# Kernel tuning notes

Measured on AMD Instinct MI355X. Metric: run time of the kernel, lower is better.

Reference implementation:

```python
import jax, jax.numpy as jnp
import numpy as np


def setup_inputs() -> dict:
    key = jax.random.key(0)
    B, M, L = 65536, 64, 256  # frames, LPC order, analysis window length
    # Build valid autocorrelation sequences (positive-definite Toeplitz)
    # from random signals via FFT: r_k = sum_t x_t x_{t+k}.
    x = jax.random.normal(key, (B, L), dtype=jnp.float32)
    spec = jnp.abs(jnp.fft.rfft(x, n=2 * L, axis=-1)) ** 2
    r = jnp.fft.irfft(spec, n=2 * L, axis=-1)[..., : M + 1] / L
    # small diagonal loading for numerical safety of the solve / sqrt
    r = r.at[..., 0].add(1e-3)
    return {"r": r.astype(jnp.float32)}


def reference(r):
    # r: (..., M+1) autocorrelation. out_format == 'Ka'.
    M = r.shape[-1] - 1
    # Symmetric Toeplitz R[i, j] = r[|i - j|] built by gathering lags.
    idx = jnp.abs(jnp.arange(M)[:, None] - jnp.arange(M)[None, :])  # (M, M)
    R = r[..., :-1][..., idx]  # (..., M, M)
    r1 = r[..., 1:]  # (..., M)
    # a = R^{-1} (-r1); solve is the efficient form of inverse @ vec (same math).
    a = jnp.linalg.solve(R, -r1[..., None])[..., 0]  # (..., M)
    r0 = r[..., 0]
    K = jnp.sqrt(jnp.einsum("...m,...m->...", r1, a) + r0)[..., None]  # (..., 1)
    return jnp.concatenate((K, a), axis=-1)  # (..., M+1)
```

## Files before the change

kernel.cpp:

```cpp
#include <hip/hip_runtime.h>
#include <math.h>


constexpr int M  = 64;
constexpr int EL = M + 1;
constexpr int BT = 128;

__global__ __launch_bounds__(BT) void levinson_kernel(const float* __restrict__ rin,
                                                      float* __restrict__ out,
                                                      int B) {
  __shared__ float smem[BT * EL];
  const int tid = threadIdx.x;
  const int b0  = blockIdx.x * BT;
  const int nb  = min(BT, B - b0);
  const int nf  = nb * EL;
  const size_t base = (size_t)b0 * EL;

  {
    const int n4 = nf >> 2;
    const float4* in4 = reinterpret_cast<const float4*>(rin + base);
    float4* s4 = reinterpret_cast<float4*>(smem);
    for (int i = tid; i < n4; i += BT) s4[i] = in4[i];
    for (int i = (n4 << 2) + tid; i < nf; i += BT) smem[i] = rin[base + i];
  }
  __syncthreads();

  float K = 0.f;
  float a[M + 1];
  if (tid < nb) {
    float r[EL];
#pragma unroll
    for (int i = 0; i < EL; ++i) r[i] = smem[tid * EL + i];

    float Eacc = r[0];
#pragma unroll
    for (int m = 1; m <= M; ++m) {
      float s[4] = {0.f, 0.f, 0.f, 0.f};
#pragma unroll
      for (int j = 1; j <= m - 1; ++j)
        s[j & 3] = fmaf(a[j], r[m - j], s[j & 3]);
      const float acc = r[m] + ((s[0] + s[1]) + (s[2] + s[3]));
      const float k = -acc / Eacc;
#pragma unroll
      for (int j = 1; 2 * j < m; ++j) {
        const float aj = a[j], amj = a[m - j];
        a[j]     = fmaf(k, amj, aj);
        a[m - j] = fmaf(k, aj, amj);
      }
      if ((m & 1) == 0) {
        const float ah = a[m >> 1];
        a[m >> 1] = fmaf(k, ah, ah);
      }
      a[m] = k;
      Eacc = fmaf(-k * k, Eacc, Eacc);
    }
    K = sqrtf(Eacc);
  }

  if (tid < nb) {
    smem[tid * EL] = K;
#pragma unroll
    for (int j = 1; j <= M; ++j) smem[tid * EL + j] = a[j];
  }
  __syncthreads();

  {
    const int n4 = nf >> 2;
    const float4* s4 = reinterpret_cast<const float4*>(smem);
    float4* out4 = reinterpret_cast<float4*>(out + base);
    for (int i = tid; i < n4; i += BT) out4[i] = s4[i];
    for (int i = (n4 << 2) + tid; i < nf; i += BT) out[base + i] = smem[i];
  }
}

extern "C" void kernel_launch(void* const* d_in, const int* in_sizes, int n_in,
                              void* d_out, int out_size, void* d_ws, size_t ws_size,
                              hipStream_t stream) {
  const float* r = (const float*)d_in[0];
  float* out = (float*)d_out;
  const int B = in_sizes[0] / EL;
  const int blocks = (B + BT - 1) / BT;
  levinson_kernel<<<blocks, BT, 0, stream>>>(r, out, B);
}
```

Measured before the change: 91.59 us.

## Reformulate Levinson recursion with fixed-length forward/backward polynomials and rolled outer loop

Replaces the triangular Levinson update, whose inner loops have lengths that depend on m and so force a full unroll of the outer loop, with a lattice formulation. It keeps a forward polynomial A and a backward polynomial Bb and runs fixed-length 64-wide dot and update loops every iteration, so the outer loop can stay rolled with register-resident arrays. This cuts instruction-cache pressure and code size, at the cost of about twice the FMAs, since each step always processes the full order instead of only m terms. The block size also drops to 64 threads with launch_bounds(…,1), which allows more registers per thread.

```diff
diff --git a/kernel.cpp b/kernel.cpp
--- a/kernel.cpp
+++ b/kernel.cpp
@@ -4,11 +4,11 @@
 
 constexpr int M  = 64;
 constexpr int EL = M + 1;
-constexpr int BT = 128;
+constexpr int BT = 64;
 
-__global__ __launch_bounds__(BT) void levinson_kernel(const float* __restrict__ rin,
-                                                      float* __restrict__ out,
-                                                      int B) {
+__global__ __launch_bounds__(BT, 1) void levinson_kernel(const float* __restrict__ rin,
+                                                         float* __restrict__ out,
+                                                         int B) {
   __shared__ float smem[BT * EL];
   const int tid = threadIdx.x;
   const int b0  = blockIdx.x * BT;
@@ -26,41 +26,50 @@
   __syncthreads();
 
   float K = 0.f;
-  float a[M + 1];
+  float A[EL];
   if (tid < nb) {
     float r[EL];
 #pragma unroll
     for (int i = 0; i < EL; ++i) r[i] = smem[tid * EL + i];
 
-    float Eacc = r[0];
+    float Bb[M];
 #pragma unroll
+    for (int i = 0; i < EL; ++i) A[i] = 0.f;
+#pragma unroll
+    for (int i = 0; i < M; ++i) Bb[i] = 0.f;
+    Bb[0] = 1.f;
+    float E = r[0];
+
+#pragma unroll 1
     for (int m = 1; m <= M; ++m) {
-      float s[4] = {0.f, 0.f, 0.f, 0.f};
+      float s0 = 0.f, s1 = 0.f, s2 = 0.f, s3 = 0.f;
 #pragma unroll
-      for (int j = 1; j <= m - 1; ++j)
-        s[j & 3] = fmaf(a[j], r[m - j], s[j & 3]);
-      const float acc = r[m] + ((s[0] + s[1]) + (s[2] + s[3]));
-      const float k = -acc / Eacc;
+      for (int i = 1; i <= M; i += 4) {
+        s0 = fmaf(Bb[i - 1], r[i],     s0);
+        s1 = fmaf(Bb[i],     r[i + 1], s1);
+        s2 = fmaf(Bb[i + 1], r[i + 2], s2);
+        s3 = fmaf(Bb[i + 2], r[i + 3], s3);
+      }
+      const float acc = (s0 + s1) + (s2 + s3);
+      const float k = -acc / E;
+
+      A[M] = fmaf(k, Bb[M - 1], A[M]);
 #pragma unroll
-      for (int j = 1; 2 * j < m; ++j) {
-        const float aj = a[j], amj = a[m - j];
-        a[j]     = fmaf(k, amj, aj);
-        a[m - j] = fmaf(k, aj, amj);
+      for (int i = M - 1; i >= 1; --i) {
+        const float tA = A[i], tb = Bb[i - 1];
+        A[i]  = fmaf(k, tb, tA);
+        Bb[i] = fmaf(k, tA, tb);
       }
-      if ((m & 1) == 0) {
-        const float ah = a[m >> 1];
-        a[m >> 1] = fmaf(k, ah, ah);
-      }
-      a[m] = k;
-      Eacc = fmaf(-k * k, Eacc, Eacc);
+      Bb[0] = k;
+      E = fmaf(-k * k, E, E);
     }
-    K = sqrtf(Eacc);
+    K = sqrtf(E);
   }
 
   if (tid < nb) {
     smem[tid * EL] = K;
 #pragma unroll
-    for (int j = 1; j <= M; ++j) smem[tid * EL + j] = a[j];
+    for (int j = 1; j <= M; ++j) smem[tid * EL + j] = A[j];
   }
   __syncthreads();
 
```

Result: slower. 106.6 us (+16.4%).

## Split each Levinson-Durbin recursion across four lanes with shuffle reductions

Applied to the files above, without the earlier changes.

Instead of one thread solving a whole 64-order Levinson-Durbin recursion, four lanes now share one frame. Each lane holds 16 coefficients plus a reversed-polynomial copy in registers, computes a partial dot product, reduces it with xor shuffles, and carries boundary values between lanes with shuffle_up. The aim is to cut the per-thread register array and serial work, raising occupancy and parallelism, at the cost of shuffles and redundant divisions each step. The partial-tile tail handling was removed, so B must be a multiple of 64 rows.

```diff
diff --git a/kernel.cpp b/kernel.cpp
--- a/kernel.cpp
+++ b/kernel.cpp
@@ -2,18 +2,21 @@
 #include <math.h>
 
 
-constexpr int M  = 64;
-constexpr int EL = M + 1;
-constexpr int BT = 128;
+constexpr int M    = 64;
+constexpr int EL   = M + 1;
+constexpr int LPB  = 4;
+constexpr int NJ   = M / LPB;
+constexpr int BT   = 256;
+constexpr int ROWS = BT / LPB;
 
-__global__ __launch_bounds__(BT) void levinson_kernel(const float* __restrict__ rin,
-                                                      float* __restrict__ out,
-                                                      int B) {
-  __shared__ float smem[BT * EL];
+__global__ __launch_bounds__(BT, 4) void levinson_kernel(const float* __restrict__ rin,
+                                                         float* __restrict__ out,
+                                                         int B) {
+  __shared__ float smem[ROWS * EL];
   const int tid = threadIdx.x;
-  const int b0  = blockIdx.x * BT;
-  const int nb  = min(BT, B - b0);
-  const int nf  = nb * EL;
+  const int b0  = blockIdx.x * ROWS;
+  if (b0 >= B) return;
+  const int nf  = ROWS * EL;
   const size_t base = (size_t)b0 * EL;
 
   {
@@ -21,46 +24,60 @@
     const float4* in4 = reinterpret_cast<const float4*>(rin + base);
     float4* s4 = reinterpret_cast<float4*>(smem);
     for (int i = tid; i < n4; i += BT) s4[i] = in4[i];
-    for (int i = (n4 << 2) + tid; i < nf; i += BT) smem[i] = rin[base + i];
   }
   __syncthreads();
 
-  float K = 0.f;
-  float a[M + 1];
-  if (tid < nb) {
-    float r[EL];
+  const int row = tid >> 2;
+  const int s   = tid & 3;
+  const float* rrow = &smem[row * EL];
+
+  float rr[NJ], aa[NJ], bb[NJ];
 #pragma unroll
-    for (int i = 0; i < EL; ++i) r[i] = smem[tid * EL + i];
+  for (int j = 0; j < NJ; ++j) rr[j] = rrow[16 * s + 1 + j];
+#pragma unroll
+  for (int j = 0; j < NJ; ++j) { aa[j] = 0.f; bb[j] = 0.f; }
+  if (s == 0) bb[0] = 1.f;
+  float E = rrow[0];
 
-    float Eacc = r[0];
+#pragma unroll 1
+  for (int m = 1; m <= M; ++m) {
+    float p0 = 0.f, p1 = 0.f, p2 = 0.f, p3 = 0.f;
 #pragma unroll
-    for (int m = 1; m <= M; ++m) {
-      float s[4] = {0.f, 0.f, 0.f, 0.f};
+    for (int j = 0; j < NJ; j += 4) {
+      p0 = fmaf(bb[j],     rr[j],     p0);
+      p1 = fmaf(bb[j + 1], rr[j + 1], p1);
+      p2 = fmaf(bb[j + 2], rr[j + 2], p2);
+      p3 = fmaf(bb[j + 3], rr[j + 3], p3);
+    }
+    float acc = (p0 + p1) + (p2 + p3);
+    acc += __shfl_xor(acc, 1);
+    acc += __shfl_xor(acc, 2);
+    const float k = -acc / E;
+
+    const float pbb = __shfl_up(bb[NJ - 1], 1);
+    const float paa = __shfl_up(aa[NJ - 1], 1);
+
 #pragma unroll
-      for (int j = 1; j <= m - 1; ++j)
-        s[j & 3] = fmaf(a[j], r[m - j], s[j & 3]);
-      const float acc = r[m] + ((s[0] + s[1]) + (s[2] + s[3]));
-      const float k = -acc / Eacc;
-#pragma unroll
-      for (int j = 1; 2 * j < m; ++j) {
-        const float aj = a[j], amj = a[m - j];
-        a[j]     = fmaf(k, amj, aj);
-        a[m - j] = fmaf(k, aj, amj);
-      }
-      if ((m & 1) == 0) {
-        const float ah = a[m >> 1];
-        a[m >> 1] = fmaf(k, ah, ah);
-      }
-      a[m] = k;
-      Eacc = fmaf(-k * k, Eacc, Eacc);
+    for (int j = NJ - 1; j >= 1; --j) {
+      const float t = bb[j];
+      bb[j] = fmaf(k, aa[j - 1], bb[j - 1]);
+      aa[j] = fmaf(k, t, aa[j]);
     }
-    K = sqrtf(Eacc);
+    {
+      const float t = bb[0];
+      bb[0] = (s == 0) ? k : fmaf(k, paa, pbb);
+      aa[0] = fmaf(k, t, aa[0]);
+    }
+    E = fmaf(-k * k, E, E);
   }
 
-  if (tid < nb) {
-    smem[tid * EL] = K;
+  __syncthreads();
+
+  {
+    float* orow = &smem[row * EL];
+    if (s == 0) orow[0] = sqrtf(E);
 #pragma unroll
-    for (int j = 1; j <= M; ++j) smem[tid * EL + j] = a[j];
+    for (int j = 0; j < NJ; ++j) orow[16 * s + 1 + j] = aa[j];
   }
   __syncthreads();
 
@@ -69,7 +86,6 @@
     const float4* s4 = reinterpret_cast<const float4*>(smem);
     float4* out4 = reinterpret_cast<float4*>(out + base);
     for (int i = tid; i < n4; i += BT) out4[i] = s4[i];
-    for (int i = (n4 << 2) + tid; i < nf; i += BT) out[base + i] = smem[i];
   }
 }
 
@@ -79,6 +95,6 @@
   const float* r = (const float*)d_in[0];
   float* out = (float*)d_out;
   const int B = in_sizes[0] / EL;
-  const int blocks = (B + BT - 1) / BT;
+  const int blocks = (B + ROWS - 1) / ROWS;
   levinson_kernel<<<blocks, BT, 0, stream>>>(r, out, B);
 }
```

After: 101.1 us. 10.3% more time.
